# Performance work log

Measured on AMD Instinct MI355X. Metric: run time of the kernel, lower is better.

## Reference

```python
import jax, jax.numpy as jnp
import numpy as np

H = 16          # heads_num
D = 1024        # model_dim
HD = D // H     # per-head dim
NEG = -1e9


def setup_inputs() -> dict:
    key = jax.random.key(0)
    ks = jax.random.split(key, 12)
    B, S = 4, 1024
    inp = {
        "q": jax.random.normal(ks[0], (B, S, D), jnp.float32),
        "k": jax.random.normal(ks[1], (B, S, D), jnp.float32),
        "v": jax.random.normal(ks[2], (B, S, D), jnp.float32),
        "mask": jnp.ones((B, 1, S), jnp.int32),
    }
    s = 1.0 / np.sqrt(D)
    inp["Wq"] = jax.random.normal(ks[3], (D, D), jnp.float32) * s
    inp["bq"] = jnp.zeros((D,), jnp.float32)
    inp["Wk"] = jax.random.normal(ks[4], (D, D), jnp.float32) * s
    inp["bk"] = jnp.zeros((D,), jnp.float32)
    inp["Wv"] = jax.random.normal(ks[5], (D, D), jnp.float32) * s
    inp["bv"] = jnp.zeros((D,), jnp.float32)
    inp["Wo"] = jax.random.normal(ks[6], (D, D), jnp.float32) * s
    inp["bo"] = jnp.zeros((D,), jnp.float32)
    return inp


def _split_heads(x, B):
    # [B, S, D] -> [B, H, S, HD]
    return x.reshape(B, -1, H, HD).transpose(0, 2, 1, 3)


def reference(q, k, v, mask, Wq, bq, Wk, bk, Wv, bv, Wo, bo):
    B = q.shape[0]
    qh = _split_heads(q @ Wq.T + bq, B)  # [B,H,Sq,HD]
    kh = _split_heads(k @ Wk.T + bk, B)  # [B,H,Sk,HD]
    vh = _split_heads(v @ Wv.T + bv, B)  # [B,H,Sk,HD]
    scores = jnp.einsum("bhqd,bhkd->bhqk", qh, kh) / np.sqrt(HD)
    # mask [B,1,Sk] -> unsqueeze head dim -> [B,1,1,Sk], broadcast over q and heads
    scores = jnp.where(mask[:, None] == 0, NEG, scores)
    attn = jax.nn.softmax(scores, axis=-1)  # dropout in eval mode = identity
    ctx = jnp.einsum("bhqk,bhkd->bhqd", attn, vh)
    out = ctx.transpose(0, 2, 1, 3).reshape(B, -1, D)
    return out @ Wo.T + bo
```

## Files before the change

kernel.cpp:

```cpp
#include <hip/hip_runtime.h>
#include <hip/hip_bf16.h>
#include <math.h>

typedef __bf16 bf16;
typedef __bf16 bf16x8 __attribute__((ext_vector_type(8)));
typedef __bf16 bf16x2 __attribute__((ext_vector_type(2)));
typedef float f32x4 __attribute__((ext_vector_type(4)));
typedef float f32x16 __attribute__((ext_vector_type(16)));

#define D_MODEL 1024
#define SEQ 1024
#define BATCH 4
#define NHEAD 16
#define MTOT (BATCH*SEQ)

#define QSCALE 0.18033688011112042f
#define MASKNEG -1e9f

__global__ void cast_w(const float* __restrict__ s0, const float* __restrict__ s1,
                       const float* __restrict__ s2, const float* __restrict__ s3,
                       bf16* d0, bf16* d1, bf16* d2, bf16* d3) {
    int z = blockIdx.y;
    const float* s; bf16* d;
    switch (z) {
        case 0: s = s0; d = d0; break;
        case 1: s = s1; d = d1; break;
        case 2: s = s2; d = d2; break;
        default: s = s3; d = d3; break;
    }
    const int n = D_MODEL * D_MODEL;
    int idx = (blockIdx.x * blockDim.x + threadIdx.x) * 8;
    int stride = gridDim.x * blockDim.x * 8;
    for (int i = idx; i < n; i += stride) {
        const float4* p = (const float4*)(s + i);
        float4 a = p[0], b = p[1];
        bf16x8 o;
        o[0] = (bf16)a.x; o[1] = (bf16)a.y; o[2] = (bf16)a.z; o[3] = (bf16)a.w;
        o[4] = (bf16)b.x; o[5] = (bf16)b.y; o[6] = (bf16)b.z; o[7] = (bf16)b.w;
        *(bf16x8*)(d + i) = o;
    }
}

__global__ __launch_bounds__(256, 3)
void gemm_qkv(const float* __restrict__ A0, const float* __restrict__ A1, const float* __restrict__ A2,
              const bf16* __restrict__ W0, const bf16* __restrict__ W1, const bf16* __restrict__ W2,
              const float* __restrict__ bias0, const float* __restrict__ bias1, const float* __restrict__ bias2,
              bf16* __restrict__ O0, bf16* __restrict__ O1, bf16* __restrict__ O2) {
    constexpr int BK = 32;
    constexpr int K = D_MODEL;
    __shared__ alignas(16) bf16 As[128 * BK];
    __shared__ alignas(16) bf16 Bs[128 * BK];

    int z = blockIdx.z;
    const float* A = (z == 0) ? A0 : (z == 1) ? A1 : A2;
    const bf16* W = (z == 0) ? W0 : (z == 1) ? W1 : W2;
    const float* bias = (z == 0) ? bias0 : (z == 1) ? bias1 : bias2;
    bf16* Out = (z == 0) ? O0 : (z == 1) ? O1 : O2;

    int tid = threadIdx.x;
    int lane = tid & 63, w = tid >> 6;
    int l15 = lane & 15, l4 = lane >> 4;
    int m0 = blockIdx.x * 128;
    int n0 = blockIdx.y * 128;
    int wm = w >> 1, wn = w & 1;

    f32x4 acc[4][4] = {};

    int srow = lane >> 2;
    int scol = (lane & 3) * 8;

    for (int k0 = 0; k0 < K; k0 += BK) {
        __syncthreads();
#pragma unroll
        for (int i = 0; i < 2; ++i) {
            int seg = w * 2 + i;
            int row = seg * 16 + srow;
            const bf16* srcB = W + (size_t)(n0 + row) * K + k0 + scol;
            __builtin_amdgcn_global_load_lds(
                (const __attribute__((address_space(1))) void*)srcB,
                (__attribute__((address_space(3))) void*)(Bs + seg * 512), 16, 0, 0);
            const float* srcA = A + (size_t)(m0 + row) * K + k0 + scol;
            float4 fa = *(const float4*)srcA;
            float4 fb = *(const float4*)(srcA + 4);
            bf16x8 o;
            o[0] = (bf16)fa.x; o[1] = (bf16)fa.y; o[2] = (bf16)fa.z; o[3] = (bf16)fa.w;
            o[4] = (bf16)fb.x; o[5] = (bf16)fb.y; o[6] = (bf16)fb.z; o[7] = (bf16)fb.w;
            *(bf16x8*)(As + seg * 512 + lane * 8) = o;
        }
        __syncthreads();

        const bf16* pa = As + (wm * 64 + l15) * BK + l4 * 8;
        const bf16* pb = Bs + (wn * 64 + l15) * BK + l4 * 8;
        bf16x8 af[4], bv[4];
#pragma unroll
        for (int m = 0; m < 4; ++m) af[m] = *(const bf16x8*)(pa + m * 16 * BK);
#pragma unroll
        for (int n = 0; n < 4; ++n) bv[n] = *(const bf16x8*)(pb + n * 16 * BK);
#pragma unroll
        for (int m = 0; m < 4; ++m)
#pragma unroll
            for (int n = 0; n < 4; ++n)
                acc[m][n] = __builtin_amdgcn_mfma_f32_16x16x32_bf16(af[m], bv[n], acc[m][n], 0, 0, 0);
    }

    float bload[4];
#pragma unroll
    for (int n = 0; n < 4; ++n) bload[n] = bias[n0 + wn * 64 + n * 16 + l15];

    if (z == 2) {
#pragma unroll
        for (int m = 0; m < 4; ++m) {
            int row = m0 + wm * 64 + m * 16 + l4 * 4;
#pragma unroll
            for (int n = 0; n < 4; ++n) {
                int col = n0 + wn * 64 + n * 16 + l15;
                float bl = bload[n];
#pragma unroll
                for (int r = 0; r < 4; ++r) {
                    float vv = acc[m][n][r] + bl;
                    int rr = row + r;
                    int bb = rr >> 10, s = rr & 1023;
                    Out[((size_t)(bb * 1024 + col)) * 1024 + s] = (bf16)vv;
                }
            }
        }
    } else {
        const float sc = (z == 0) ? QSCALE : 1.0f;
#pragma unroll
        for (int m = 0; m < 4; ++m) {
            int row = m0 + wm * 64 + m * 16 + l4 * 4;
#pragma unroll
            for (int n = 0; n < 4; ++n) {
                int col = n0 + wn * 64 + n * 16 + l15;
                float bl = bload[n];
#pragma unroll
                for (int r = 0; r < 4; ++r) {
                    float vv = (acc[m][n][r] + bl) * sc;
                    Out[(size_t)(row + r) * D_MODEL + col] = (bf16)vv;
                }
            }
        }
    }
}

__global__ __launch_bounds__(256, 3)
void gemm_out(const bf16* __restrict__ A, const bf16* __restrict__ W,
              const float* __restrict__ bias, float* __restrict__ Out) {
    constexpr int BK = 32;
    constexpr int K = D_MODEL;
    __shared__ alignas(16) bf16 As[128 * BK];
    __shared__ alignas(16) bf16 Bs[128 * BK];

    int tid = threadIdx.x;
    int lane = tid & 63, w = tid >> 6;
    int l15 = lane & 15, l4 = lane >> 4;
    int m0 = blockIdx.x * 128;
    int n0 = blockIdx.y * 128;
    int wm = w >> 1, wn = w & 1;

    f32x4 acc[4][4] = {};
    int srow = lane >> 2;
    int scol = (lane & 3) * 8;

    for (int k0 = 0; k0 < K; k0 += BK) {
        __syncthreads();
#pragma unroll
        for (int i = 0; i < 2; ++i) {
            int seg = w * 2 + i;
            int row = seg * 16 + srow;
            const bf16* srcA = A + (size_t)(m0 + row) * K + k0 + scol;
            const bf16* srcB = W + (size_t)(n0 + row) * K + k0 + scol;
            __builtin_amdgcn_global_load_lds(
                (const __attribute__((address_space(1))) void*)srcA,
                (__attribute__((address_space(3))) void*)(As + seg * 512), 16, 0, 0);
            __builtin_amdgcn_global_load_lds(
                (const __attribute__((address_space(1))) void*)srcB,
                (__attribute__((address_space(3))) void*)(Bs + seg * 512), 16, 0, 0);
        }
        __syncthreads();

        const bf16* pa = As + (wm * 64 + l15) * BK + l4 * 8;
        const bf16* pb = Bs + (wn * 64 + l15) * BK + l4 * 8;
        bf16x8 af[4], bv[4];
#pragma unroll
        for (int m = 0; m < 4; ++m) af[m] = *(const bf16x8*)(pa + m * 16 * BK);
#pragma unroll
        for (int n = 0; n < 4; ++n) bv[n] = *(const bf16x8*)(pb + n * 16 * BK);
#pragma unroll
        for (int m = 0; m < 4; ++m)
#pragma unroll
            for (int n = 0; n < 4; ++n)
                acc[m][n] = __builtin_amdgcn_mfma_f32_16x16x32_bf16(af[m], bv[n], acc[m][n], 0, 0, 0);
    }

    float bload[4];
#pragma unroll
    for (int n = 0; n < 4; ++n) bload[n] = bias[n0 + wn * 64 + n * 16 + l15];
#pragma unroll
    for (int m = 0; m < 4; ++m) {
        int row = m0 + wm * 64 + m * 16 + l4 * 4;
#pragma unroll
        for (int n = 0; n < 4; ++n) {
            int col = n0 + wn * 64 + n * 16 + l15;
            float bl = bload[n];
#pragma unroll
            for (int r = 0; r < 4; ++r)
                Out[(size_t)(row + r) * D_MODEL + col] = acc[m][n][r] + bl;
        }
    }
}

__device__ __forceinline__ unsigned pkbf(float lo, float hi2) {
    bf16x2 t; t[0] = (bf16)lo; t[1] = (bf16)hi2;
    return __builtin_bit_cast(unsigned, t);
}

__global__ __launch_bounds__(512, 2)
void attn_fwd(const bf16* __restrict__ Qp, const bf16* __restrict__ Kp,
              const bf16* __restrict__ VT, const int* __restrict__ maskp,
              bf16* __restrict__ ctx) {
    __shared__ alignas(16) bf16 Kls[2][64 * 64];
    __shared__ alignas(16) bf16 Vls[2][64 * 64];
    __shared__ alignas(16) float madd2[SEQ];
    __shared__ int tflag[16];

    int tid = threadIdx.x;
    int lane = tid & 63, w = tid >> 6;
    int l31 = lane & 31, hi = lane >> 5;

    int fid = blockIdx.x;
    int xcd = fid & 7, idx = fid >> 3;
    int by = xcd * 8 + (idx >> 2);
    int bx = idx & 3;
    int b = by >> 4, h = by & 15;
    int q0 = bx * 256;

    {
        int m0v = maskp[b * SEQ + tid];
        int m1v = maskp[b * SEQ + 512 + tid];
        madd2[tid] = m0v ? 0.f : MASKNEG;
        madd2[512 + tid] = m1v ? 0.f : MASKNEG;
        unsigned long long b0 = __ballot(m0v != 0);
        unsigned long long b1 = __ballot(m1v != 0);
        if (lane == 0) {
            tflag[w] = (b0 == ~0ull);
            tflag[8 + w] = (b1 == ~0ull);
        }
    }

    bf16x8 qf[4];
    {
        const bf16* qb = Qp + ((size_t)(b * SEQ + q0 + w * 32 + l31)) * D_MODEL + h * 64 + hi * 8;
#pragma unroll
        for (int ks = 0; ks < 4; ++ks) qf[ks] = *(const bf16x8*)(qb + ks * 16);
    }

    f32x16 oacc0 = {}, oacc1 = {};
    float lsum = 0.f;

    auto stage = [&](int buf, int kt) {
        int kv0 = kt * 64;
        int row = w * 8 + (lane >> 3);
        int cs = ((lane & 7) ^ (row & 7)) * 8;
        const bf16* srcK = Kp + ((size_t)(b * SEQ + kv0 + row)) * D_MODEL + h * 64 + cs;
        __builtin_amdgcn_global_load_lds(
            (const __attribute__((address_space(1))) void*)srcK,
            (__attribute__((address_space(3))) void*)(&Kls[buf][w * 512]), 16, 0, 0);
        const bf16* srcV = VT + ((size_t)(b * 1024 + h * 64 + row)) * SEQ + kv0 + cs;
        __builtin_amdgcn_global_load_lds(
            (const __attribute__((address_space(1))) void*)srcV,
            (__attribute__((address_space(3))) void*)(&Vls[buf][w * 512]), 16, 0, 0);
    };

    stage(0, 0);
    __syncthreads();

    for (int kt = 0; kt < SEQ / 64; ++kt) {
        int cur = kt & 1;
        if (kt + 1 < SEQ / 64) stage(cur ^ 1, kt + 1);

        f32x16 p0 = {}, p1 = {};
        __builtin_amdgcn_s_setprio(1);
#pragma unroll
        for (int ks = 0; ks < 4; ++ks) {
            int slot = ((2 * ks + hi) ^ (l31 & 7)) * 8;
            bf16x8 k0 = *(const bf16x8*)(&Kls[cur][l31 * 64 + slot]);
            bf16x8 k1 = *(const bf16x8*)(&Kls[cur][(32 + l31) * 64 + slot]);
            p0 = __builtin_amdgcn_mfma_f32_32x32x16_bf16(k0, qf[ks], p0, 0, 0, 0);
            p1 = __builtin_amdgcn_mfma_f32_32x32x16_bf16(k1, qf[ks], p1, 0, 0, 0);
        }
        __builtin_amdgcn_s_setprio(0);

        float a0 = 0.f, a1 = 0.f, a2 = 0.f, a3 = 0.f;
        if (tflag[kt]) {
#pragma unroll
            for (int g = 0; g < 4; ++g) {
                float s0 = 0.f, s1 = 0.f;
#pragma unroll
                for (int c = 0; c < 4; ++c) {
                    int r = g * 4 + c;
                    float e0 = exp2f(p0[r]);
                    float e1 = exp2f(p1[r]);
                    p0[r] = e0; p1[r] = e1;
                    s0 += e0; s1 += e1;
                }
                if (g == 0) a0 = s0 + s1;
                else if (g == 1) a1 = s0 + s1;
                else if (g == 2) a2 = s0 + s1;
                else a3 = s0 + s1;
            }
        } else {
            const float* mb = &madd2[kt * 64];
#pragma unroll
            for (int g = 0; g < 4; ++g) {
                f32x4 mk0 = *(const f32x4*)(mb + g * 8 + hi * 4);
                f32x4 mk1 = *(const f32x4*)(mb + 32 + g * 8 + hi * 4);
                float s0 = 0.f, s1 = 0.f;
#pragma unroll
                for (int c = 0; c < 4; ++c) {
                    int r = g * 4 + c;
                    float e0 = exp2f(p0[r] + mk0[c]);
                    float e1 = exp2f(p1[r] + mk1[c]);
                    p0[r] = e0; p1[r] = e1;
                    s0 += e0; s1 += e1;
                }
                if (g == 0) a0 = s0 + s1;
                else if (g == 1) a1 = s0 + s1;
                else if (g == 2) a2 = s0 + s1;
                else a3 = s0 + s1;
            }
        }
        float acc_s = (a0 + a1) + (a2 + a3);
        acc_s += __shfl_xor(acc_s, 32);
        lsum += acc_s;

        union FragU { bf16x8 v; unsigned u[4]; };
        FragU pa0, pa1, pa2, pa3;
#define PKSW(PV, RA, RB, DST)  { \
            unsigned a_ = pkbf(PV[RA], PV[(RA) + 1]); \
            unsigned b_ = pkbf(PV[RB], PV[(RB) + 1]); \
            auto rr_ = __builtin_amdgcn_permlane32_swap(a_, b_, false, false); \
            DST.u[((RA) & 3) >> 1] = rr_[0]; DST.u[(((RA) & 3) >> 1) + 2] = rr_[1]; }
        PKSW(p0, 0, 4,  pa0);
        PKSW(p0, 2, 6,  pa0);
        PKSW(p0, 8, 12, pa1);
        PKSW(p0, 10, 14, pa1);
        PKSW(p1, 0, 4,  pa2);
        PKSW(p1, 2, 6,  pa2);
        PKSW(p1, 8, 12, pa3);
        PKSW(p1, 10, 14, pa3);
#undef PKSW

        __builtin_amdgcn_s_setprio(1);
#pragma unroll
        for (int ks = 0; ks < 4; ++ks) {
            bf16x8 pav = (ks == 0) ? pa0.v : (ks == 1) ? pa1.v : (ks == 2) ? pa2.v : pa3.v;
            int slot = ((2 * ks + hi) ^ (l31 & 7)) * 8;
            bf16x8 v0 = *(const bf16x8*)(&Vls[cur][l31 * 64 + slot]);
            bf16x8 v1 = *(const bf16x8*)(&Vls[cur][(32 + l31) * 64 + slot]);
            oacc0 = __builtin_amdgcn_mfma_f32_32x32x16_bf16(pav, v0, oacc0, 0, 0, 0);
            oacc1 = __builtin_amdgcn_mfma_f32_32x32x16_bf16(pav, v1, oacc1, 0, 0, 0);
        }
        __builtin_amdgcn_s_setprio(0);

        __syncthreads();
    }

#pragma unroll
    for (int g = 0; g < 4; ++g) {
#pragma unroll
        for (int c = 0; c < 4; ++c) {
            int r = g * 4 + c;
            int qloc = c + g * 8 + hi * 4;
            float sden = __shfl(lsum, qloc);
            float inv = 1.0f / sden;
            int qg = q0 + w * 32 + qloc;
            size_t base = ((size_t)(b * SEQ + qg)) * D_MODEL + h * 64;
            ctx[base + l31]      = (bf16)(oacc0[r] * inv);
            ctx[base + 32 + l31] = (bf16)(oacc1[r] * inv);
        }
    }
}

extern "C" void kernel_launch(void* const* d_in, const int* in_sizes, int n_in,
                              void* d_out, int out_size, void* d_ws, size_t ws_size,
                              hipStream_t stream) {
    const float* q  = (const float*)d_in[0];
    const float* k  = (const float*)d_in[1];
    const float* v  = (const float*)d_in[2];
    const int* mask = (const int*)d_in[3];
    const float* Wq = (const float*)d_in[4];
    const float* bq = (const float*)d_in[5];
    const float* Wk = (const float*)d_in[6];
    const float* bk = (const float*)d_in[7];
    const float* Wv = (const float*)d_in[8];
    const float* bv = (const float*)d_in[9];
    const float* Wo = (const float*)d_in[10];
    const float* bo = (const float*)d_in[11];
    float* out = (float*)d_out;

    char* ws = (char*)d_ws;
    size_t szQKV = (size_t)MTOT * D_MODEL * sizeof(bf16);
    size_t szW = (size_t)D_MODEL * D_MODEL * sizeof(bf16);
    bf16* Wqb = (bf16*)ws; ws += szW;
    bf16* Wkb = (bf16*)ws; ws += szW;
    bf16* Wvb = (bf16*)ws; ws += szW;
    bf16* Wob = (bf16*)ws; ws += szW;
    bf16* Qp  = (bf16*)ws; ws += szQKV;
    bf16* Kp  = (bf16*)ws; ws += szQKV;
    bf16* VT  = (bf16*)ws; ws += szQKV;
    bf16* ctx = (bf16*)ws; ws += szQKV;

    dim3 gc(256, 4, 1);
    cast_w<<<gc, 256, 0, stream>>>(Wq, Wk, Wv, Wo, Wqb, Wkb, Wvb, Wob);

    dim3 g1(MTOT / 128, D_MODEL / 128, 3);
    gemm_qkv<<<g1, 256, 0, stream>>>(q, k, v, Wqb, Wkb, Wvb,
                                     bq, bk, bv, Qp, Kp, VT);

    attn_fwd<<<dim3(256), 512, 0, stream>>>(Qp, Kp, VT, mask, ctx);

    dim3 g3(MTOT / 128, D_MODEL / 128, 1);
    gemm_out<<<g3, 256, 0, stream>>>(ctx, Wob, bo, out);
}
```

Measured before the change: 111.1 us.

## Double-buffer LDS tiles in QKV projection GEMM with register-prefetched A

Converts the QKV projection GEMM main loop to a two-stage software pipeline. The next W tile is loaded asynchronously into the alternate LDS buffer, and the next fp32 A tile is prefetched into registers while the current tile's MFMAs run. The A tile is then converted to bf16 and written to LDS after the MFMAs, leaving one barrier per iteration instead of two. The cost is twice the LDS footprint and more live registers, which may reduce occupancy under the 3-blocks-per-CU launch bound.

```diff
diff --git a/kernel.cpp b/kernel.cpp
--- a/kernel.cpp
+++ b/kernel.cpp
@@ -48,8 +48,9 @@
               bf16* __restrict__ O0, bf16* __restrict__ O1, bf16* __restrict__ O2) {
     constexpr int BK = 32;
     constexpr int K = D_MODEL;
-    __shared__ alignas(16) bf16 As[128 * BK];
-    __shared__ alignas(16) bf16 Bs[128 * BK];
+    constexpr int NT = K / BK;
+    __shared__ alignas(16) bf16 As[2][128 * BK];
+    __shared__ alignas(16) bf16 Bs[2][128 * BK];
 
     int z = blockIdx.z;
     const float* A = (z == 0) ? A0 : (z == 1) ? A1 : A2;
@@ -66,31 +67,59 @@
 
     f32x4 acc[4][4] = {};
 
+    int arow = tid >> 2;
+    int acol = (tid & 3) * 8;
+    const float* aBase = A + (size_t)(m0 + arow) * K + acol;
     int srow = lane >> 2;
     int scol = (lane & 3) * 8;
 
-    for (int k0 = 0; k0 < K; k0 += BK) {
-        __syncthreads();
+    float4 fa0, fa1, fb0, fb1;
+
+    auto loadA = [&](int kt) {
+        const float* p0 = aBase + kt * BK;
+        const float* p1 = p0 + (size_t)64 * K;
+        fa0 = *(const float4*)p0;
+        fa1 = *(const float4*)(p0 + 4);
+        fb0 = *(const float4*)p1;
+        fb1 = *(const float4*)(p1 + 4);
+    };
+    auto writeA = [&](int buf) {
+        bf16x8 o;
+        o[0] = (bf16)fa0.x; o[1] = (bf16)fa0.y; o[2] = (bf16)fa0.z; o[3] = (bf16)fa0.w;
+        o[4] = (bf16)fa1.x; o[5] = (bf16)fa1.y; o[6] = (bf16)fa1.z; o[7] = (bf16)fa1.w;
+        *(bf16x8*)(&As[buf][arow * BK + acol]) = o;
+        bf16x8 p;
+        p[0] = (bf16)fb0.x; p[1] = (bf16)fb0.y; p[2] = (bf16)fb0.z; p[3] = (bf16)fb0.w;
+        p[4] = (bf16)fb1.x; p[5] = (bf16)fb1.y; p[6] = (bf16)fb1.z; p[7] = (bf16)fb1.w;
+        *(bf16x8*)(&As[buf][(arow + 64) * BK + acol]) = p;
+    };
+    auto stageW = [&](int buf, int kt) {
 #pragma unroll
         for (int i = 0; i < 2; ++i) {
             int seg = w * 2 + i;
             int row = seg * 16 + srow;
-            const bf16* srcB = W + (size_t)(n0 + row) * K + k0 + scol;
+            const bf16* srcB = W + (size_t)(n0 + row) * K + kt * BK + scol;
             __builtin_amdgcn_global_load_lds(
                 (const __attribute__((address_space(1))) void*)srcB,
-                (__attribute__((address_space(3))) void*)(Bs + seg * 512), 16, 0, 0);
-            const float* srcA = A + (size_t)(m0 + row) * K + k0 + scol;
-            float4 fa = *(const float4*)srcA;
-            float4 fb = *(const float4*)(srcA + 4);
-            bf16x8 o;
-            o[0] = (bf16)fa.x; o[1] = (bf16)fa.y; o[2] = (bf16)fa.z; o[3] = (bf16)fa.w;
-            o[4] = (bf16)fb.x; o[5] = (bf16)fb.y; o[6] = (bf16)fb.z; o[7] = (bf16)fb.w;
-            *(bf16x8*)(As + seg * 512 + lane * 8) = o;
-        }
-        __syncthreads();
-
-        const bf16* pa = As + (wm * 64 + l15) * BK + l4 * 8;
-        const bf16* pb = Bs + (wn * 64 + l15) * BK + l4 * 8;
+                (__attribute__((address_space(3))) void*)(&Bs[buf][seg * 512]), 16, 0, 0);
+        }
+    };
+
+    stageW(0, 0);
+    loadA(0);
+    writeA(0);
+    __syncthreads();
+
+    for (int kt = 0; kt < NT; ++kt) {
+        int cur = kt & 1;
+        bool pre = (kt + 1 < NT);
+        if (pre) {
+            stageW(cur ^ 1, kt + 1);
+            loadA(kt + 1);
+        }
+
+        const bf16* pa = &As[cur][(wm * 64 + l15) * BK + l4 * 8];
+        const bf16* pb = &Bs[cur][(wn * 64 + l15) * BK + l4 * 8];
         bf16x8 af[4], bv[4];
 #pragma unroll
         for (int m = 0; m < 4; ++m) af[m] = *(const bf16x8*)(pa + m * 16 * BK);
@@ -101,6 +130,9 @@
 #pragma unroll
             for (int n = 0; n < 4; ++n)
                 acc[m][n] = __builtin_amdgcn_mfma_f32_16x16x32_bf16(af[m], bv[n], acc[m][n], 0, 0, 0);
+
+        if (pre) writeA(cur ^ 1);
+        __syncthreads();
     }
 
     float bload[4];
```

New measurement: 111.7 us. No clear change (+0.5%).
